# Kernel optimization log

Measured on AMD Instinct MI355X. Metric: run time of the kernel, lower is better.

Reference implementation:

```python
import jax, jax.numpy as jnp
import numpy as np

V = 50000
E = 800000
B, CIN, COUT, K = 4, 64, 128, 4


def setup_inputs() -> dict:
    key = jax.random.key(0)
    k1, k2, k3, k4, k5 = jax.random.split(key, 5)
    x = jax.random.normal(k1, (B, CIN, V), dtype=jnp.float32)
    lap_rows = jnp.sort(jax.random.randint(k2, (E,), 0, V, dtype=jnp.int32))
    lap_cols = jax.random.randint(k3, (E,), 0, V, dtype=jnp.int32)
    # scale ~1/sqrt(avg_degree) so recurrence stays bounded (laplacian-like spectrum)
    lap_vals = jax.random.normal(k4, (E,), dtype=jnp.float32) * (1.0 / np.sqrt(16.0))
    # kaiming init per module: std = sqrt(2/(Cin*K))
    weight = jax.random.normal(k5, (K, CIN, COUT), dtype=jnp.float32) * np.sqrt(2.0 / (CIN * K))
    bias = jnp.full((COUT,), 0.01, dtype=jnp.float32)
    return {"x": x, "lap_rows": lap_rows, "lap_cols": lap_cols,
            "lap_vals": lap_vals, "weight": weight, "bias": bias}


def reference(x, lap_rows, lap_cols, lap_vals, weight, bias):
    # x: (B, Cin, V); laplacian sparse COO (rows, cols, vals); weight: (K, Cin, Cout)
    Bn, Cin, Vn = x.shape
    Kn = weight.shape[0]

    def spmm(z):  # z: (V, B*Cin) -> laplacian @ z
        return jax.ops.segment_sum(lap_vals[:, None] * z[lap_cols], lap_rows,
                                   num_segments=Vn)

    def contract(z, w):  # (V, B*Cin) x (Cin, Cout) -> (V, B, Cout)
        return jnp.einsum('vbi,io->vbo', z.reshape(Vn, Bn, Cin), w)

    x0 = jnp.transpose(x, (2, 0, 1)).reshape(Vn, Bn * Cin)
    # fused Chebyshev recurrence: accumulate weight contraction per step
    out = contract(x0, weight[0])
    if Kn > 1:
        x1 = spmm(x0)
        out = out + contract(x1, weight[1])
        for k in range(2, Kn):
            x2 = 2.0 * spmm(x1) - x0
            out = out + contract(x2, weight[k])
            x0, x1 = x1, x2
    out = out + bias  # broadcast over (V, B, Cout)
    return jnp.transpose(out, (1, 2, 0))  # (B, Cout, V)
```

## Files before the change

kernel.cpp:

```cpp
#include <hip/hip_runtime.h>
#include <hip/hip_bf16.h>

#define VN 50000
#define EN 800000
#define BN 4
#define CINN 64
#define COUTN 128
#define KN 4
#define FN 256

typedef __attribute__((ext_vector_type(8))) short short8;
typedef __attribute__((ext_vector_type(8))) unsigned short ushort8;
typedef __attribute__((ext_vector_type(4))) float floatx4;

__device__ __forceinline__ float bf2f(unsigned short u) {
    union { unsigned int i; float f; } c;
    c.i = ((unsigned int)u) << 16;
    return c.f;
}
__device__ __forceinline__ unsigned short f2bf(float f) {
    __hip_bfloat16 h = __float2bfloat16(f);
    return *reinterpret_cast<unsigned short*>(&h);
}

#define RP_BLOCKS 196
#define WT_BLOCKS 128
#define TP_BX 782
#define TP_BLOCKS (TP_BX * 4)

__global__ __launch_bounds__(256) void setup_fused(const int* __restrict__ rows,
                                                   int* __restrict__ row_ptr,
                                                   const float* __restrict__ w,
                                                   ushort* __restrict__ wT,
                                                   const float* __restrict__ x,
                                                   ushort* __restrict__ x0) {
    __shared__ float tile[64][65];
    int blk = blockIdx.x;
    int tid = threadIdx.x;
    if (blk < RP_BLOCKS) {
        int v = blk * 256 + tid;
        if (v > VN) return;
        int lo = 0, hi = EN;
        while (lo < hi) {
            int mid = (lo + hi) >> 1;
            if (rows[mid] < v) lo = mid + 1; else hi = mid;
        }
        row_ptr[v] = lo;
        return;
    }
    if (blk < RP_BLOCKS + WT_BLOCKS) {
        int idx = (blk - RP_BLOCKS) * 256 + tid;
        int o = idx >> 8;
        int kk = idx & 255;
        wT[idx] = f2bf(w[(size_t)kk * COUTN + o]);
        return;
    }
    int t = blk - RP_BLOCKS - WT_BLOCKS;
    int v0 = (t % TP_BX) * 64;
    int f0 = (t / TP_BX) * 64;
    int tx = tid & 63;
    int ty = tid >> 6;
#pragma unroll
    for (int r = 0; r < 16; ++r) {
        int f = f0 + ty + r * 4;
        int v = v0 + tx;
        if (v < VN) tile[ty + r * 4][tx] = x[(size_t)f * VN + v];
    }
    __syncthreads();
#pragma unroll
    for (int r = 0; r < 16; ++r) {
        int v = v0 + ty + r * 4;
        int f = f0 + tx;
        if (v < VN) x0[(size_t)v * FN + f] = f2bf(tile[tx][ty + r * 4]);
    }
}

__global__ __launch_bounds__(256) void spmm_cheb_bf16(ushort* __restrict__ out,
                                                      const ushort* __restrict__ z,
                                                      const ushort* __restrict__ prev,
                                                      const int* __restrict__ row_ptr,
                                                      const int* __restrict__ cols,
                                                      const float* __restrict__ vals,
                                                      float alpha, float beta) {
    int row = (int)((blockIdx.x * blockDim.x + threadIdx.x) >> 6);
    int lane = threadIdx.x & 63;
    if (row >= VN) return;
    int e0 = row_ptr[row];
    int e1 = row_ptr[row + 1];
    int half = lane >> 5;
    int fl = (lane & 31) * 8;

    float acc0[8], acc1[8];
#pragma unroll
    for (int j = 0; j < 8; ++j) { acc0[j] = 0.f; acc1[j] = 0.f; }

    int e = e0 + half;
    for (; e + 6 < e1; e += 8) {
        int c0 = cols[e], c1 = cols[e + 2], c2 = cols[e + 4], c3 = cols[e + 6];
        float w0 = vals[e], w1 = vals[e + 2], w2 = vals[e + 4], w3 = vals[e + 6];
        ushort8 z0 = *reinterpret_cast<const ushort8*>(z + (size_t)c0 * FN + fl);
        ushort8 z1 = *reinterpret_cast<const ushort8*>(z + (size_t)c1 * FN + fl);
        ushort8 z2 = *reinterpret_cast<const ushort8*>(z + (size_t)c2 * FN + fl);
        ushort8 z3 = *reinterpret_cast<const ushort8*>(z + (size_t)c3 * FN + fl);
#pragma unroll
        for (int j = 0; j < 8; ++j) acc0[j] += w0 * bf2f(z0[j]);
#pragma unroll
        for (int j = 0; j < 8; ++j) acc1[j] += w1 * bf2f(z1[j]);
#pragma unroll
        for (int j = 0; j < 8; ++j) acc0[j] += w2 * bf2f(z2[j]);
#pragma unroll
        for (int j = 0; j < 8; ++j) acc1[j] += w3 * bf2f(z3[j]);
    }
    for (; e + 2 < e1; e += 4) {
        int c0 = cols[e], c1 = cols[e + 2];
        float w0 = vals[e], w1 = vals[e + 2];
        ushort8 z0 = *reinterpret_cast<const ushort8*>(z + (size_t)c0 * FN + fl);
        ushort8 z1 = *reinterpret_cast<const ushort8*>(z + (size_t)c1 * FN + fl);
#pragma unroll
        for (int j = 0; j < 8; ++j) acc0[j] += w0 * bf2f(z0[j]);
#pragma unroll
        for (int j = 0; j < 8; ++j) acc1[j] += w1 * bf2f(z1[j]);
    }
    for (; e < e1; e += 2) {
        int c0 = cols[e];
        float w0 = vals[e];
        ushort8 z0 = *reinterpret_cast<const ushort8*>(z + (size_t)c0 * FN + fl);
#pragma unroll
        for (int j = 0; j < 8; ++j) acc0[j] += w0 * bf2f(z0[j]);
    }
#pragma unroll
    for (int j = 0; j < 8; ++j) acc0[j] += acc1[j];
#pragma unroll
    for (int j = 0; j < 8; ++j) acc0[j] += __shfl(acc0[j], lane ^ 32);

    if (half == 0) {
        ushort8 pv = *reinterpret_cast<const ushort8*>(prev + (size_t)row * FN + fl);
        ushort8 res;
#pragma unroll
        for (int j = 0; j < 8; ++j)
            res[j] = f2bf(alpha * acc0[j] + beta * bf2f(pv[j]));
        *reinterpret_cast<ushort8*>(out + (size_t)row * FN + fl) = res;
    }
}

__global__ __launch_bounds__(256) void cheb_gemm_mfma(float* __restrict__ out,
                                                      const ushort* __restrict__ xbase,
                                                      const ushort* __restrict__ wT,
                                                      const float* __restrict__ bias) {
    __shared__ __align__(16) short lsA[128 * 64];
    __shared__ __align__(16) short lsB[128 * 64];

    int b = blockIdx.y;
    int v0 = blockIdx.x * 128;
    int tid = threadIdx.x;
    int lane = tid & 63;
    int w = tid >> 6;
    int mw = w & 1;
    int nw = w >> 1;
    int ln = lane & 15;
    int quad = lane >> 4;

    int srow = tid >> 1;
    int posBase = (tid & 1) * 4;

    floatx4 acc[4][4];
#pragma unroll
    for (int mi = 0; mi < 4; ++mi)
#pragma unroll
        for (int ni = 0; ni < 4; ++ni) acc[mi][ni] = (floatx4){0.f, 0.f, 0.f, 0.f};

    for (int kc = 0; kc < 4; ++kc) {
        __syncthreads();
#pragma unroll
        for (int j = 0; j < 4; ++j) {
            int pos = posBase + j;
            int g = pos ^ (srow & 7);
            uint4 val = *reinterpret_cast<const uint4*>(wT + (size_t)srow * 256 + kc * 64 + g * 8);
            *reinterpret_cast<uint4*>(&lsA[(srow * 8 + pos) * 8]) = val;
        }
        {
            const ushort* xk = xbase + (size_t)kc * VN * FN;
            int v = v0 + srow;
            bool ok = (v < VN);
            const ushort* src = xk + (size_t)v * FN + b * CINN;
#pragma unroll
            for (int j = 0; j < 4; ++j) {
                int pos = posBase + j;
                int g = pos ^ (srow & 7);
                uint4 val;
                if (ok) val = *reinterpret_cast<const uint4*>(src + g * 8);
                else    val = make_uint4(0u, 0u, 0u, 0u);
                *reinterpret_cast<uint4*>(&lsB[(srow * 8 + pos) * 8]) = val;
            }
        }
        __syncthreads();

#pragma unroll
        for (int s = 0; s < 2; ++s) {
            short8 afr[4], bfr[4];
#pragma unroll
            for (int mi = 0; mi < 4; ++mi) {
                int r = mw * 64 + mi * 16 + ln;
                int pos = (s * 4 + quad) ^ (r & 7);
                afr[mi] = *reinterpret_cast<const short8*>(&lsA[(r * 8 + pos) * 8]);
            }
#pragma unroll
            for (int ni = 0; ni < 4; ++ni) {
                int r = nw * 64 + ni * 16 + ln;
                int pos = (s * 4 + quad) ^ (r & 7);
                bfr[ni] = *reinterpret_cast<const short8*>(&lsB[(r * 8 + pos) * 8]);
            }
#pragma unroll
            for (int mi = 0; mi < 4; ++mi)
#pragma unroll
                for (int ni = 0; ni < 4; ++ni)
                    acc[mi][ni] = __builtin_amdgcn_mfma_f32_16x16x32_bf16(
                        afr[mi], bfr[ni], acc[mi][ni], 0, 0, 0);
        }
    }

#pragma unroll
    for (int mi = 0; mi < 4; ++mi) {
#pragma unroll
        for (int r = 0; r < 4; ++r) {
            int o = mw * 64 + mi * 16 + quad * 4 + r;
            float bv = bias[o];
            size_t obase = (size_t)(b * COUTN + o) * VN;
#pragma unroll
            for (int ni = 0; ni < 4; ++ni) {
                int v = v0 + nw * 64 + ni * 16 + ln;
                if (v < VN) out[obase + v] = acc[mi][ni][r] + bv;
            }
        }
    }
}

extern "C" void kernel_launch(void* const* d_in, const int* in_sizes, int n_in,
                              void* d_out, int out_size, void* d_ws, size_t ws_size,
                              hipStream_t stream) {
    const float* x        = (const float*)d_in[0];
    const int*   lap_rows = (const int*)d_in[1];
    const int*   lap_cols = (const int*)d_in[2];
    const float* lap_vals = (const float*)d_in[3];
    const float* weight   = (const float*)d_in[4];
    const float* bias     = (const float*)d_in[5];
    float* out = (float*)d_out;

    char* ws = (char*)d_ws;
    ushort* x0 = (ushort*)ws;
    ushort* x1 = x0 + (size_t)VN * FN;
    ushort* x2 = x1 + (size_t)VN * FN;
    ushort* x3 = x2 + (size_t)VN * FN;
    size_t xbytes = (size_t)4 * VN * FN * sizeof(ushort);
    int* row_ptr = (int*)(ws + xbytes);
    size_t rp_end = xbytes + (size_t)(VN + 1) * sizeof(int);
    rp_end = (rp_end + 15) & ~(size_t)15;
    ushort* wT = (ushort*)(ws + rp_end);

    setup_fused<<<RP_BLOCKS + WT_BLOCKS + TP_BLOCKS, 256, 0, stream>>>(
        lap_rows, row_ptr, weight, wT, x, x0);
    spmm_cheb_bf16<<<(VN + 3) / 4, 256, 0, stream>>>(x1, x0, x0, row_ptr, lap_cols, lap_vals, 1.f, 0.f);
    spmm_cheb_bf16<<<(VN + 3) / 4, 256, 0, stream>>>(x2, x1, x0, row_ptr, lap_cols, lap_vals, 2.f, -1.f);
    spmm_cheb_bf16<<<(VN + 3) / 4, 256, 0, stream>>>(x3, x2, x1, row_ptr, lap_cols, lap_vals, 2.f, -1.f);
    cheb_gemm_mfma<<<dim3((VN + 127) / 128, BN), 256, 0, stream>>>(out, x0, wT, bias);
}
```

Baseline: 373.4 us.

## Slice feature layout into 32-wide panels and pack edge col/val pairs

Stores the Chebyshev feature buffers in a sliced layout (8 panels of 32 features, each V x 32), so each SpMM block handles one panel and its gathers touch a smaller working set that fits better in cache. Column indices and values are packed into 64-bit words in setup so each edge needs one load, and those loads plus the output stores use nontemporal hints. The GEMM loader is adjusted to read the new layout. The cost is that edge metadata is now re-read once per slice (eight times per step) and the gathers become 64-byte segments instead of full 512-byte rows.

```diff
diff --git a/kernel.cpp b/kernel.cpp
--- a/kernel.cpp
+++ b/kernel.cpp
@@ -12,6 +12,7 @@
 typedef __attribute__((ext_vector_type(8))) short short8;
 typedef __attribute__((ext_vector_type(8))) unsigned short ushort8;
 typedef __attribute__((ext_vector_type(4))) float floatx4;
+typedef unsigned int uintx4 __attribute__((ext_vector_type(4)));
 
 __device__ __forceinline__ float bf2f(unsigned short u) {
     union { unsigned int i; float f; } c;
@@ -25,15 +26,20 @@
 
 #define RP_BLOCKS 196
 #define WT_BLOCKS 128
+#define EP_BLOCKS 3125
 #define TP_BX 782
 #define TP_BLOCKS (TP_BX * 4)
+#define SPMM_BLOCKS (TP_BX * 8)
 
 __global__ __launch_bounds__(256) void setup_fused(const int* __restrict__ rows,
                                                    int* __restrict__ row_ptr,
                                                    const float* __restrict__ w,
                                                    ushort* __restrict__ wT,
                                                    const float* __restrict__ x,
-                                                   ushort* __restrict__ x0) {
+                                                   ushort* __restrict__ x0,
+                                                   const int* __restrict__ cols,
+                                                   const float* __restrict__ vals,
+                                                   unsigned long long* __restrict__ epack) {
     __shared__ float tile[64][65];
     int blk = blockIdx.x;
     int tid = threadIdx.x;
@@ -55,7 +61,14 @@
         wT[idx] = f2bf(w[(size_t)kk * COUTN + o]);
         return;
     }
-    int t = blk - RP_BLOCKS - WT_BLOCKS;
+    if (blk < RP_BLOCKS + WT_BLOCKS + EP_BLOCKS) {
+        int idx = (blk - RP_BLOCKS - WT_BLOCKS) * 256 + tid;
+        unsigned int c = (unsigned int)cols[idx];
+        unsigned int wv = __float_as_uint(vals[idx]);
+        epack[idx] = ((unsigned long long)wv << 32) | (unsigned long long)c;
+        return;
+    }
+    int t = blk - RP_BLOCKS - WT_BLOCKS - EP_BLOCKS;
     int v0 = (t % TP_BX) * 64;
     int f0 = (t / TP_BX) * 64;
     int tx = tid & 63;
@@ -71,76 +84,81 @@
     for (int r = 0; r < 16; ++r) {
         int v = v0 + ty + r * 4;
         int f = f0 + tx;
-        if (v < VN) x0[(size_t)v * FN + f] = f2bf(tile[tx][ty + r * 4]);
-    }
-}
-
-__global__ __launch_bounds__(256) void spmm_cheb_bf16(ushort* __restrict__ out,
-                                                      const ushort* __restrict__ z,
-                                                      const ushort* __restrict__ prev,
-                                                      const int* __restrict__ row_ptr,
-                                                      const int* __restrict__ cols,
-                                                      const float* __restrict__ vals,
-                                                      float alpha, float beta) {
-    int row = (int)((blockIdx.x * blockDim.x + threadIdx.x) >> 6);
-    int lane = threadIdx.x & 63;
-    if (row >= VN) return;
-    int e0 = row_ptr[row];
-    int e1 = row_ptr[row + 1];
-    int half = lane >> 5;
-    int fl = (lane & 31) * 8;
-
-    float acc0[8], acc1[8];
-#pragma unroll
-    for (int j = 0; j < 8; ++j) { acc0[j] = 0.f; acc1[j] = 0.f; }
-
-    int e = e0 + half;
-    for (; e + 6 < e1; e += 8) {
-        int c0 = cols[e], c1 = cols[e + 2], c2 = cols[e + 4], c3 = cols[e + 6];
-        float w0 = vals[e], w1 = vals[e + 2], w2 = vals[e + 4], w3 = vals[e + 6];
-        ushort8 z0 = *reinterpret_cast<const ushort8*>(z + (size_t)c0 * FN + fl);
-        ushort8 z1 = *reinterpret_cast<const ushort8*>(z + (size_t)c1 * FN + fl);
-        ushort8 z2 = *reinterpret_cast<const ushort8*>(z + (size_t)c2 * FN + fl);
-        ushort8 z3 = *reinterpret_cast<const ushort8*>(z + (size_t)c3 * FN + fl);
-#pragma unroll
-        for (int j = 0; j < 8; ++j) acc0[j] += w0 * bf2f(z0[j]);
-#pragma unroll
-        for (int j = 0; j < 8; ++j) acc1[j] += w1 * bf2f(z1[j]);
-#pragma unroll
-        for (int j = 0; j < 8; ++j) acc0[j] += w2 * bf2f(z2[j]);
-#pragma unroll
-        for (int j = 0; j < 8; ++j) acc1[j] += w3 * bf2f(z3[j]);
-    }
-    for (; e + 2 < e1; e += 4) {
-        int c0 = cols[e], c1 = cols[e + 2];
-        float w0 = vals[e], w1 = vals[e + 2];
-        ushort8 z0 = *reinterpret_cast<const ushort8*>(z + (size_t)c0 * FN + fl);
-        ushort8 z1 = *reinterpret_cast<const ushort8*>(z + (size_t)c1 * FN + fl);
-#pragma unroll
-        for (int j = 0; j < 8; ++j) acc0[j] += w0 * bf2f(z0[j]);
-#pragma unroll
-        for (int j = 0; j < 8; ++j) acc1[j] += w1 * bf2f(z1[j]);
-    }
-    for (; e < e1; e += 2) {
-        int c0 = cols[e];
-        float w0 = vals[e];
-        ushort8 z0 = *reinterpret_cast<const ushort8*>(z + (size_t)c0 * FN + fl);
-#pragma unroll
-        for (int j = 0; j < 8; ++j) acc0[j] += w0 * bf2f(z0[j]);
-    }
-#pragma unroll
-    for (int j = 0; j < 8; ++j) acc0[j] += acc1[j];
-#pragma unroll
-    for (int j = 0; j < 8; ++j) acc0[j] += __shfl(acc0[j], lane ^ 32);
-
-    if (half == 0) {
-        ushort8 pv = *reinterpret_cast<const ushort8*>(prev + (size_t)row * FN + fl);
-        ushort8 res;
-#pragma unroll
-        for (int j = 0; j < 8; ++j)
-            res[j] = f2bf(alpha * acc0[j] + beta * bf2f(pv[j]));
-        *reinterpret_cast<ushort8*>(out + (size_t)row * FN + fl) = res;
-    }
+        if (v < VN)
+            x0[((size_t)(f >> 5) * VN + v) * 32 + (f & 31)] = f2bf(tile[tx][ty + r * 4]);
+    }
+}
+
+__global__ __launch_bounds__(256) void spmm_sliced(ushort* __restrict__ out,
+                                                   const ushort* __restrict__ z,
+                                                   const ushort* __restrict__ prev,
+                                                   const int* __restrict__ row_ptr,
+                                                   const unsigned long long* __restrict__ epack,
+                                                   float alpha, float beta) {
+    int bid = blockIdx.x;
+    int s = bid & 7;
+    int rb = bid >> 3;
+    int tid = threadIdx.x;
+    int lane = tid & 63;
+    int g = lane >> 2;
+    int l = lane & 3;
+    int r = rb * 64 + (tid >> 6) * 16 + g;
+    if (r >= VN) return;
+
+    const ushort* zs = z + (size_t)s * VN * 32 + l * 8;
+    int e0 = row_ptr[r];
+    int e1 = row_ptr[r + 1];
+
+    float acc[8], acc2[8];
+#pragma unroll
+    for (int j = 0; j < 8; ++j) { acc[j] = 0.f; acc2[j] = 0.f; }
+
+    int e = e0;
+    for (; e + 3 < e1; e += 4) {
+        unsigned long long d0 = __builtin_nontemporal_load(epack + e);
+        unsigned long long d1 = __builtin_nontemporal_load(epack + e + 1);
+        unsigned long long d2 = __builtin_nontemporal_load(epack + e + 2);
+        unsigned long long d3 = __builtin_nontemporal_load(epack + e + 3);
+        ushort8 z0 = *reinterpret_cast<const ushort8*>(zs + (size_t)(unsigned int)d0 * 32);
+        ushort8 z1 = *reinterpret_cast<const ushort8*>(zs + (size_t)(unsigned int)d1 * 32);
+        ushort8 z2 = *reinterpret_cast<const ushort8*>(zs + (size_t)(unsigned int)d2 * 32);
+        ushort8 z3 = *reinterpret_cast<const ushort8*>(zs + (size_t)(unsigned int)d3 * 32);
+        float w0 = __uint_as_float((unsigned int)(d0 >> 32));
+        float w1 = __uint_as_float((unsigned int)(d1 >> 32));
+        float w2 = __uint_as_float((unsigned int)(d2 >> 32));
+        float w3 = __uint_as_float((unsigned int)(d3 >> 32));
+#pragma unroll
+        for (int j = 0; j < 8; ++j) acc[j] += w0 * bf2f(z0[j]);
+#pragma unroll
+        for (int j = 0; j < 8; ++j) acc2[j] += w1 * bf2f(z1[j]);
+#pragma unroll
+        for (int j = 0; j < 8; ++j) acc[j] += w2 * bf2f(z2[j]);
+#pragma unroll
+        for (int j = 0; j < 8; ++j) acc2[j] += w3 * bf2f(z3[j]);
+    }
+    for (; e < e1; ++e) {
+        unsigned long long d = __builtin_nontemporal_load(epack + e);
+        ushort8 zz = *reinterpret_cast<const ushort8*>(zs + (size_t)(unsigned int)d * 32);
+        float w = __uint_as_float((unsigned int)(d >> 32));
+#pragma unroll
+        for (int j = 0; j < 8; ++j) acc[j] += w * bf2f(zz[j]);
+    }
+#pragma unroll
+    for (int j = 0; j < 8; ++j) acc[j] += acc2[j];
+
+    size_t off = ((size_t)s * VN + r) * 32 + l * 8;
+    ushort8 res;
+    if (beta != 0.f) {
+        ushort8 pv = *reinterpret_cast<const ushort8*>(prev + off);
+#pragma unroll
+        for (int j = 0; j < 8; ++j) res[j] = f2bf(alpha * acc[j] + beta * bf2f(pv[j]));
+    } else {
+#pragma unroll
+        for (int j = 0; j < 8; ++j) res[j] = f2bf(alpha * acc[j]);
+    }
+    union { ushort8 u; uintx4 v; } cvt;
+    cvt.u = res;
+    __builtin_nontemporal_store(cvt.v, reinterpret_cast<uintx4*>(out + off));
 }
 
 __global__ __launch_bounds__(256) void cheb_gemm_mfma(float* __restrict__ out,
@@ -182,13 +200,14 @@
             const ushort* xk = xbase + (size_t)kc * VN * FN;
             int v = v0 + srow;
             bool ok = (v < VN);
-            const ushort* src = xk + (size_t)v * FN + b * CINN;
 #pragma unroll
             for (int j = 0; j < 4; ++j) {
                 int pos = posBase + j;
                 int g = pos ^ (srow & 7);
+                int p = b * 2 + (g >> 2);
+                const ushort* src = xk + ((size_t)p * VN + v) * 32 + (g & 3) * 8;
                 uint4 val;
-                if (ok) val = *reinterpret_cast<const uint4*>(src + g * 8);
+                if (ok) val = *reinterpret_cast<const uint4*>(src);
                 else    val = make_uint4(0u, 0u, 0u, 0u);
                 *reinterpret_cast<uint4*>(&lsB[(srow * 8 + pos) * 8]) = val;
             }
@@ -256,11 +275,12 @@
     size_t rp_end = xbytes + (size_t)(VN + 1) * sizeof(int);
     rp_end = (rp_end + 15) & ~(size_t)15;
     ushort* wT = (ushort*)(ws + rp_end);
-
-    setup_fused<<<RP_BLOCKS + WT_BLOCKS + TP_BLOCKS, 256, 0, stream>>>(
-        lap_rows, row_ptr, weight, wT, x, x0);
-    spmm_cheb_bf16<<<(VN + 3) / 4, 256, 0, stream>>>(x1, x0, x0, row_ptr, lap_cols, lap_vals, 1.f, 0.f);
-    spmm_cheb_bf16<<<(VN + 3) / 4, 256, 0, stream>>>(x2, x1, x0, row_ptr, lap_cols, lap_vals, 2.f, -1.f);
-    spmm_cheb_bf16<<<(VN + 3) / 4, 256, 0, stream>>>(x3, x2, x1, row_ptr, lap_cols, lap_vals, 2.f, -1.f);
+    unsigned long long* epack = (unsigned long long*)(ws + rp_end + (size_t)COUTN * FN * sizeof(ushort));
+
+    setup_fused<<<RP_BLOCKS + WT_BLOCKS + EP_BLOCKS + TP_BLOCKS, 256, 0, stream>>>(
+        lap_rows, row_ptr, weight, wT, x, x0, lap_cols, lap_vals, epack);
+    spmm_sliced<<<SPMM_BLOCKS, 256, 0, stream>>>(x1, x0, x0, row_ptr, epack, 1.f, 0.f);
+    spmm_sliced<<<SPMM_BLOCKS, 256, 0, stream>>>(x2, x1, x0, row_ptr, epack, 2.f, -1.f);
+    spmm_sliced<<<SPMM_BLOCKS, 256, 0, stream>>>(x3, x2, x1, row_ptr, epack, 2.f, -1.f);
     cheb_gemm_mfma<<<dim3((VN + 127) / 128, BN), 256, 0, stream>>>(out, x0, wT, bias);
 }
```

Measured after the change: 519.2 us. +39.1%, slower.
